# Optimization experiments

Measured on AMD Instinct MI355X. Metric: run time of the kernel, lower is better.

## Reference

```python
import jax, jax.numpy as jnp
import numpy as np

T, N, F = 8, 10000, 16
E, H, LD, ENVD = 320000, 64, 3, 5
TEMP, SAL, UI, VI = 11, 12, 13, 14
ENV_IDX = jnp.array([11, 12, 13, 14, 15])
DECAY_KM = 15.0


def _lin(k, o, i, s=0.1):
    return jax.random.normal(k, (o, i), jnp.float32) * s


def setup_inputs() -> dict:
    key = jax.random.key(0)
    ks = jax.random.split(key, 24)
    inp = {
        'node_features_sequence': jax.random.normal(ks[0], (T, N, F), jnp.float32),
        'initial_lice': jax.random.uniform(ks[1], (N, LD), jnp.float32),
        'edge_distance': jax.random.uniform(ks[2], (E,), jnp.float32) * 30.0,
        'edge_direction': jax.random.normal(ks[3], (E, 2), jnp.float32),
        'ee_w1': _lin(ks[4], H, 4), 'ee_b1': jnp.zeros((H,)),
        'ee_w2': _lin(ks[5], H, H), 'ee_b2': jnp.zeros((H,)),
        'at_w1': _lin(ks[6], H, 2 * H), 'at_b1': jnp.zeros((H,)),
        'at_w2': _lin(ks[7], 1, H), 'at_b2': jnp.zeros((1,)),
        'en_w1': _lin(ks[8], H, ENVD), 'en_b1': jnp.zeros((H,)),
        'en_w2': _lin(ks[9], H, H), 'en_b2': jnp.zeros((H,)),
        'fe_w1': _lin(ks[10], 32, 1), 'fe_b1': jnp.zeros((32,)),
        'fe_w2': _lin(ks[11], 32, 32), 'fe_b2': jnp.zeros((32,)),
        'fe_w3': _lin(ks[12], 1, 32), 'fe_b3': jnp.zeros((1,)),
        'gru_wih': _lin(ks[13], 3 * H, H + ENVD + LD),
        'gru_whh': _lin(ks[14], 3 * H, H),
        'gru_bih': jnp.zeros((3 * H,)), 'gru_bhh': jnp.zeros((3 * H,)),
        'de_w1': _lin(ks[15], H, H), 'de_b1': jnp.zeros((H,)),
        'de_w2': _lin(ks[16], LD, H), 'de_b2': jnp.zeros((LD,)),
        'log_beta': jnp.float32(-1.0),
        'temp_sensitivity': jnp.float32(0.1),
        'edge_index': jax.random.randint(ks[17], (2, E), 0, N, jnp.int32),
    }
    return inp


def _mlp2(x, w1, b1, w2, b2):
    return jax.nn.relu(x @ w1.T + b1) @ w2.T + b2


def _gru(x, h, wih, whh, bih, bhh):
    gi = x @ wih.T + bih
    gh = h @ whh.T + bhh
    i_r, i_z, i_n = jnp.split(gi, 3, axis=-1)
    h_r, h_z, h_n = jnp.split(gh, 3, axis=-1)
    r = jax.nn.sigmoid(i_r + h_r)
    z = jax.nn.sigmoid(i_z + h_z)
    n = jnp.tanh(i_n + r * h_n)
    return (1.0 - z) * n + z * h


def reference(node_features_sequence, initial_lice, edge_distance, edge_direction,
              ee_w1, ee_b1, ee_w2, ee_b2, at_w1, at_b1, at_w2, at_b2,
              en_w1, en_b1, en_w2, en_b2, fe_w1, fe_b1, fe_w2, fe_b2, fe_w3, fe_b3,
              gru_wih, gru_whh, gru_bih, gru_bhh, de_w1, de_b1, de_w2, de_b2,
              log_beta, temp_sensitivity, edge_index):
    src, dst = edge_index[0], edge_index[1]
    dist_factor = jnp.exp(-edge_distance / DECAY_KM)
    beta = jnp.exp(log_beta)

    def step(carry, x_t):
        h, lice = carry
        # dynamic edge attributes: [distance, flux+ * decay, temp_src, sal_src]
        u = x_t[src, UI]
        v = x_t[src, VI]
        flux = u * edge_direction[:, 0] + v * edge_direction[:, 1]
        wflux = jnp.clip(flux, 0.0) * dist_factor
        edge_attr = jnp.stack([edge_distance, wflux, x_t[src, TEMP], x_t[src, SAL]], axis=1)
        # edge MLP + attention logits  (E,H)
        ef = _mlp2(edge_attr, ee_w1, ee_b1, ee_w2, ee_b2)
        h_src = h[src]
        logits = _mlp2(jnp.concatenate([ef, h_src], axis=-1), at_w1, at_b1, at_w2, at_b2)[:, 0]
        logits = logits + jnp.log(wflux + 1e-8)
        # per-destination segment softmax
        amax = jax.ops.segment_max(logits, dst, num_segments=N)
        aexp = jnp.exp(logits - amax[dst])
        asum = jax.ops.segment_sum(aexp, dst, num_segments=N)
        aw = aexp / (asum[dst] + 1e-8)
        # flux-weighted lice messages, scatter-add to destinations
        weighted = (aw * lice[src, 0] * beta)[:, None] * h_src  # (E,H)
        pressure = jax.ops.segment_sum(weighted, dst, num_segments=N)  # (N,H)
        # environment + fecundity
        env = x_t[:, ENV_IDX]
        temp_norm = (x_t[:, TEMP] - 10.0) / 5.0
        fec = jax.nn.softplus(
            _mlp2(jax.nn.relu(temp_norm[:, None] @ fe_w1.T + fe_b1), fe_w2, fe_b2, fe_w3, fe_b3))[:, 0]
        env_enc = _mlp2(env, en_w1, en_b1, en_w2, en_b2)
        din = jnp.concatenate([env_enc + pressure, env, lice], axis=-1)
        h_new = _gru(din, h, gru_wih, gru_whh, gru_bih, gru_bhh)
        lice_base = jax.nn.softplus(_mlp2(h_new, de_w1, de_b1, de_w2, de_b2))
        lice_new = lice_base * (1.0 + temp_sensitivity * (fec[:, None] - 1.0))
        return (h_new, lice_new), lice_new

    h0 = jnp.zeros((N, H), jnp.float32)
    _, traj = jax.lax.scan(step, (h0, initial_lice), node_features_sequence)
    return traj  # (T, N, feature_dim)
```

## Files before the change

### kernel.cpp

```cpp
#include <hip/hip_runtime.h>
#include <math.h>

#define T_STEPS 8
#define NNODES 10000
#define NFEAT 16
#define NEDGES 320000
#define HDIM 64
#define LDIM 3
#define CAP 128

typedef _Float16 f16x8 __attribute__((ext_vector_type(8)));
typedef _Float16 f16x4 __attribute__((ext_vector_type(4)));
typedef float f32x4 __attribute__((ext_vector_type(4)));

__device__ __forceinline__ float sigmoidf_(float x){ return 1.f/(1.f+__expf(-x)); }
__device__ __forceinline__ float softplusf_(float x){ return fmaxf(x,0.f)+log1pf(__expf(-fabsf(x))); }
__device__ __forceinline__ float tanhf_(float x){ return 2.f*sigmoidf_(2.f*x)-1.f; }


__global__ void __launch_bounds__(256) k_prep(
    const float* __restrict__ ee_w2, const float* __restrict__ ee_b2,
    const float* __restrict__ at_w1, const float* __restrict__ at_b1,
    _Float16* __restrict__ P_Mhi, _Float16* __restrict__ P_Mlo,
    float* __restrict__ cvec)
{
    int i = blockIdx.x*256 + threadIdx.x;
    if (i >= 64*64) return;
    int m = i>>6, j = i&63;
    float acc = 0.f;
    #pragma unroll 8
    for (int k=0;k<64;++k) acc += ee_w2[k*64+m]*at_w1[j*128+k];
    int ks = m>>5;
    int lane = ((m>>3)&3)*16 + (j&15);
    int elem = m&7;
    int fi = (j>>4)*2 + ks;
    _Float16 hi = (_Float16)acc;
    P_Mhi[(fi*64+lane)*8+elem] = hi;
    P_Mlo[(fi*64+lane)*8+elem] = (_Float16)(acc - (float)hi);
    if (m == 0){
        float c = at_b1[j];
        #pragma unroll 8
        for (int k=0;k<64;++k) c += ee_b2[k]*at_w1[j*128+k];
        cvec[j] = c;
    }
}

__device__ __forceinline__ void packB(const float* __restrict__ W, int ldw, int koff, int K, int NKS,
                                      _Float16* __restrict__ Dhi, _Float16* __restrict__ Dlo, int li){
    int elem = li & 7;
    int lane = (li >> 3) & 63;
    int fi   = li >> 9;
    int jt = fi / NKS, ks = fi % NKS;
    int j = jt*16 + (lane & 15);
    int k = ks*32 + ((lane>>4)&3)*8 + elem;
    float v = (k < K) ? W[j*ldw + koff + k] : 0.f;
    _Float16 hi = (_Float16)v;
    Dhi[li] = hi;
    Dlo[li] = (_Float16)(v - (float)hi);
}

__global__ void __launch_bounds__(256) k_init(
    const float* __restrict__ init_lice, const float* __restrict__ cvec,
    const float* __restrict__ en_w1, const float* __restrict__ en_w2,
    const float* __restrict__ gru_wih, const float* __restrict__ gru_whh,
    const float* __restrict__ de_w1, const float* __restrict__ at_w1,
    float* __restrict__ h, float* __restrict__ lice, float* __restrict__ G,
    _Float16* __restrict__ F_en1h, _Float16* __restrict__ F_en1l,
    _Float16* __restrict__ F_enh,  _Float16* __restrict__ F_enl,
    _Float16* __restrict__ F_ihh,  _Float16* __restrict__ F_ihl,
    _Float16* __restrict__ F_hhh,  _Float16* __restrict__ F_hhl,
    _Float16* __restrict__ F_deh,  _Float16* __restrict__ F_del,
    _Float16* __restrict__ F_a2h,  _Float16* __restrict__ F_a2l,
    int* __restrict__ counts)
{
    int i = blockIdx.x*256 + threadIdx.x;
    if (i < NNODES*HDIM){ h[i] = 0.f; G[i] = cvec[i&63]; }
    if (i < NNODES*LDIM) lice[i] = init_lice[i];
    if (i < NNODES) counts[i] = 0;
    if (i < 2048)       packB(en_w1,   5,  0,  5, 1, F_en1h, F_en1l, i);
    else if (i < 6144)  packB(en_w2,  64,  0, 64, 2, F_enh,  F_enl,  i-2048);
    else if (i < 24576) packB(gru_wih,72,  0, 72, 3, F_ihh,  F_ihl,  i-6144);
    else if (i < 36864) packB(gru_whh,64,  0, 64, 2, F_hhh,  F_hhl,  i-24576);
    else if (i < 40960) packB(de_w1,  64,  0, 64, 2, F_deh,  F_del,  i-36864);
    else if (i < 45056) packB(at_w1, 128, 64, 64, 2, F_a2h,  F_a2l,  i-40960);
}

__global__ void __launch_bounds__(256) k_fec(
    const float* __restrict__ nfs,
    const float* __restrict__ fe_w1, const float* __restrict__ fe_b1,
    const float* __restrict__ fe_w2, const float* __restrict__ fe_b2,
    const float* __restrict__ fe_w3, const float* __restrict__ fe_b3,
    float* __restrict__ fec_arr)
{
    int i = blockIdx.x*256 + threadIdx.x;
    if (i >= T_STEPS*NNODES) return;
    float temp = nfs[(size_t)i*NFEAT + 11];
    float tn = (temp - 10.f)*(1.f/5.f);
    float a[32];
    #pragma unroll
    for (int k=0;k<32;++k) a[k] = fmaxf(tn*fe_w1[k] + fe_b1[k], 0.f);
    float o = fe_b3[0];
    #pragma unroll 4
    for (int l=0;l<32;++l){
        float b = fe_b2[l];
        #pragma unroll
        for (int k=0;k<32;++k) b += a[k]*fe_w2[l*32+k];
        o += fmaxf(b, 0.f)*fe_w3[l];
    }
    fec_arr[i] = softplusf_(o);
}

__global__ void __launch_bounds__(256) k_hist(const int* __restrict__ ei_dst, int* __restrict__ counts){
    int e = blockIdx.x*256 + threadIdx.x;
    if (e < NEDGES) atomicAdd(&counts[ei_dst[e]], 1);
}

__global__ void __launch_bounds__(1024) k_scan(const int* __restrict__ counts,
                                               int* __restrict__ rowptr, int* __restrict__ cursor){
    __shared__ int sums[1024];
    int t = threadIdx.x;
    const int CH = 10;
    int c0 = t*CH;
    int s = 0;
    if (c0 < NNODES){
        #pragma unroll
        for (int i=0;i<CH;i++) s += counts[c0+i];
    }
    sums[t] = s;
    __syncthreads();
    for (int off=1; off<1024; off<<=1){
        int v = (t>=off) ? sums[t-off] : 0;
        __syncthreads();
        sums[t] += v;
        __syncthreads();
    }
    if (c0 < NNODES){
        int run = (t==0) ? 0 : sums[t-1];
        for (int i=0;i<CH;i++){ rowptr[c0+i] = run; run += counts[c0+i]; cursor[c0+i] = 0; }
        if (t == (NNODES/CH)-1) rowptr[NNODES] = run;
    }
}

__global__ void __launch_bounds__(256) k_scatter(const int* __restrict__ ei_dst,
        const int* __restrict__ rowptr, int* __restrict__ cursor, int* __restrict__ perm){
    int e = blockIdx.x*256 + threadIdx.x;
    if (e >= NEDGES) return;
    int d = ei_dst[e];
    int pos = rowptr[d] + atomicAdd(&cursor[d], 1);
    perm[pos] = e;
}

__global__ void __launch_bounds__(256) k_permg(
    const int* __restrict__ perm, const int* __restrict__ ei_src,
    const float* __restrict__ dist, const float* __restrict__ dirn,
    int* __restrict__ src_perm, float* __restrict__ dist_p, float* __restrict__ dirn_p)
{
    int i = blockIdx.x*256 + threadIdx.x;
    if (i >= NEDGES) return;
    int e = perm[i];
    src_perm[i] = ei_src[e];
    dist_p[i] = dist[e];
    float2 dd = *reinterpret_cast<const float2*>(dirn + 2*e);
    *reinterpret_cast<float2*>(dirn_p + 2*i) = dd;
}


__global__ void __launch_bounds__(256,2) k_edge_mfma(
    const float* __restrict__ xt, const float* __restrict__ G,
    const int* __restrict__ src_perm,
    const float* __restrict__ dist_p, const float* __restrict__ dirn_p,
    const float* __restrict__ ee_w1, const float* __restrict__ ee_b1,
    const _Float16* __restrict__ P_Mhi, const _Float16* __restrict__ P_Mlo,
    const float* __restrict__ at_w2, const float* __restrict__ at_b2,
    float* __restrict__ logits)
{
    __shared__ __align__(16) _Float16 smh[36864];
    float* smf = (float*)smh;

    const int tid = threadIdx.x;
    const int wv = tid>>6, lane = tid&63;
    const int e = blockIdx.x*256 + tid;

    f16x8 bh[4][2], bl[4][2];
    #pragma unroll
    for (int jt=0;jt<4;++jt){
        #pragma unroll
        for (int ks=0;ks<2;++ks){
            bh[jt][ks] = *(const f16x8*)(P_Mhi + (((jt*2+ks)*64 + lane)*8));
            bl[jt][ks] = *(const f16x8*)(P_Mlo + (((jt*2+ks)*64 + lane)*8));
        }
    }

    const int src = src_perm[e];
    const float d  = dist_p[e];
    float2 dir2 = *reinterpret_cast<const float2*>(dirn_p + 2*e);
    float temp = xt[src*NFEAT+11];
    float4 q  = *reinterpret_cast<const float4*>(xt + src*NFEAT + 12);
    float flux = q.y*dir2.x + q.z*dir2.y;
    float wflux = fmaxf(flux, 0.f) * __expf(-d*(1.f/15.f));
    const float a0 = d, a1 = wflux, a2 = temp, a3 = q.x;
    const float lbias = at_b2[0] + __logf(wflux + 1e-8f);

    #pragma unroll
    for (int kb=0;kb<8;++kb){
        f16x8 hv, lv;
        #pragma unroll
        for (int i=0;i<8;++i){
            const int m = kb*8+i;
            float4 w1 = *reinterpret_cast<const float4*>(ee_w1 + m*4);
            float r = fmaxf(ee_b1[m] + a0*w1.x + a1*w1.y + a2*w1.z + a3*w1.w, 0.f);
            _Float16 hi = (_Float16)r;
            hv[i] = hi;
            lv[i] = (_Float16)(r - (float)hi);
        }
        *(f16x8*)(smh + tid*72 + kb*8)         = hv;
        *(f16x8*)(smh + 18432 + tid*72 + kb*8) = lv;
    }
    asm volatile("s_waitcnt lgkmcnt(0)" ::: "memory");

    f32x4 c[4][4];
    #pragma unroll
    for (int et=0;et<4;++et)
        #pragma unroll
        for (int jt=0;jt<4;++jt)
            c[et][jt] = (f32x4){0.f,0.f,0.f,0.f};

    #pragma unroll
    for (int et=0;et<4;++et){
        #pragma unroll
        for (int ks=0;ks<2;++ks){
            const int row = wv*64 + et*16 + (lane&15);
            f16x8 ah = *(const f16x8*)(smh + row*72 + ks*32 + (lane>>4)*8);
            f16x8 al = *(const f16x8*)(smh + 18432 + row*72 + ks*32 + (lane>>4)*8);
            #pragma unroll
            for (int jt=0;jt<4;++jt){
                c[et][jt] = __builtin_amdgcn_mfma_f32_16x16x32_f16(ah, bh[jt][ks], c[et][jt], 0,0,0);
                c[et][jt] = __builtin_amdgcn_mfma_f32_16x16x32_f16(ah, bl[jt][ks], c[et][jt], 0,0,0);
                c[et][jt] = __builtin_amdgcn_mfma_f32_16x16x32_f16(al, bh[jt][ks], c[et][jt], 0,0,0);
            }
        }
    }
    asm volatile("s_waitcnt lgkmcnt(0)" ::: "memory");

    #pragma unroll
    for (int et=0;et<4;++et){
        #pragma unroll
        for (int jt=0;jt<4;++jt){
            #pragma unroll
            for (int i=0;i<4;++i){
                const int rl = et*16 + ((lane>>4)&3)*4 + i;
                const int col = jt*16 + (lane&15);
                const int idx = (et < 2) ? (wv*2304 + rl*68 + col)
                                         : (9216 + wv*2304 + (rl-32)*68 + col);
                smf[idx] = c[et][jt][i];
            }
        }
    }
    asm volatile("s_waitcnt lgkmcnt(0)" ::: "memory");

    const int el = tid & 63;
    const float* crow = smf + ((el < 32) ? (wv*2304 + el*68)
                                         : (9216 + wv*2304 + (el-32)*68));
    const float4* G4 = reinterpret_cast<const float4*>(G + src*HDIM);
    float logit = lbias;
    #pragma unroll
    for (int jj=0;jj<16;++jj){
        float4 cv = *reinterpret_cast<const float4*>(crow + jj*4);
        float4 gv = G4[jj];
        float4 w4 = *reinterpret_cast<const float4*>(at_w2 + jj*4);
        logit += w4.x*fmaxf(cv.x+gv.x,0.f) + w4.y*fmaxf(cv.y+gv.y,0.f)
               + w4.z*fmaxf(cv.z+gv.z,0.f) + w4.w*fmaxf(cv.w+gv.w,0.f);
    }
    logits[e] = logit;
}


__global__ void __launch_bounds__(256) k_softmax_pressure(
    const float* __restrict__ logits, const float* __restrict__ h,
    const float* __restrict__ lice, const int* __restrict__ src_perm,
    const int* __restrict__ rowptr,
    const float* __restrict__ log_beta,
    float* __restrict__ pressure)
{
    __shared__ float swgt[CAP];
    __shared__ int   ssrc[CAP];
    __shared__ float sred[4][64];
    __shared__ float sredm[4], sreds[4];

    const int node = blockIdx.x;
    const int tid = threadIdx.x;
    const int wid = tid >> 6;
    const int lane = tid & 63;
    const int start = rowptr[node], end = rowptr[node+1];
    const int deg = end - start;
    const int nfast = deg < CAP ? deg : CAP;

    float m = -INFINITY;
    for (int i=start+tid; i<end; i+=256){
        float lg = logits[i];
        int o = i - start;
        if (o < CAP){ swgt[o] = lg; ssrc[o] = src_perm[i]; }
        m = fmaxf(m, lg);
    }
    #pragma unroll
    for (int off=32; off>=1; off>>=1) m = fmaxf(m, __shfl_xor(m, off));
    if (lane == 0) sredm[wid] = m;
    __syncthreads();
    m = fmaxf(fmaxf(sredm[0], sredm[1]), fmaxf(sredm[2], sredm[3]));

    float s = 0.f;
    for (int i=start+tid; i<end; i+=256){
        int o = i - start;
        float lg = (o < CAP) ? swgt[o] : logits[i];
        s += __expf(lg - m);
    }
    #pragma unroll
    for (int off=32; off>=1; off>>=1) s += __shfl_xor(s, off);
    if (lane == 0) sreds[wid] = s;
    __syncthreads();
    s = (sreds[0]+sreds[1])+(sreds[2]+sreds[3]);

    const float binv = __expf(log_beta[0])/(s + 1e-8f);

    for (int o=tid; o<nfast; o+=256){
        int sc = ssrc[o];
        swgt[o] = __expf(swgt[o] - m) * binv * lice[sc*LDIM];
    }
    __syncthreads();

    float p = 0.f;
    for (int o=wid; o<nfast; o+=4)
        p += swgt[o]*h[ssrc[o]*HDIM + lane];
    for (int i=start+CAP+wid; i<end; i+=4){
        int sc = src_perm[i];
        float wg = __expf(logits[i]-m)*binv*lice[sc*LDIM];
        p += wg*h[sc*HDIM+lane];
    }
    sred[wid][lane] = p;
    __syncthreads();
    if (wid == 0)
        pressure[node*HDIM + lane] = (sred[0][lane]+sred[1][lane])+(sred[2][lane]+sred[3][lane]);
}


__global__ void __launch_bounds__(256,4) k_node_mfma(
    const float* __restrict__ xt,
    float* __restrict__ h, float* __restrict__ lice,
    const float* __restrict__ pressure,
    const _Float16* __restrict__ F_en1h, const _Float16* __restrict__ F_en1l,
    const _Float16* __restrict__ F_enh,  const _Float16* __restrict__ F_enl,
    const _Float16* __restrict__ F_ihh,  const _Float16* __restrict__ F_ihl,
    const _Float16* __restrict__ F_hhh,  const _Float16* __restrict__ F_hhl,
    const _Float16* __restrict__ F_deh,  const _Float16* __restrict__ F_del,
    const _Float16* __restrict__ F_a2h,  const _Float16* __restrict__ F_a2l,
    const float* __restrict__ en_b1, const float* __restrict__ en_b2,
    const float* __restrict__ gru_bih, const float* __restrict__ gru_bhh,
    const float* __restrict__ de_b1, const float* __restrict__ de_w2, const float* __restrict__ de_b2,
    const float* __restrict__ cvec, const float* __restrict__ fec_t,
    const float* __restrict__ temp_sens,
    float* __restrict__ G, float* __restrict__ out_t)
{
    __shared__ __align__(16) _Float16 Ah_hi[16*72], Ah_lo[16*72];
    __shared__ __align__(16) _Float16 At_hi[16*72], At_lo[16*72];
    __shared__ __align__(16) _Float16 Ad_hi[16*104], Ad_lo[16*104];
    __shared__ float s_pd[16*64];
    __shared__ float s_fec[16];

    const int tid = threadIdx.x;
    const int w = tid>>6, lane = tid&63;
    const int l15 = lane & 15, lq = (lane>>4)&3;
    const int n0 = blockIdx.x*16;

    {
        int node = tid>>4, k4 = tid&15;
        int nc = n0 + node;
        float4 hv = *reinterpret_cast<const float4*>(h + nc*64 + k4*4);
        float4 pv = *reinterpret_cast<const float4*>(pressure + nc*64 + k4*4);
        *reinterpret_cast<float4*>(s_pd + node*64 + k4*4) = pv;
        f16x4 hh, hl;
        hh[0]=(_Float16)hv.x; hh[1]=(_Float16)hv.y; hh[2]=(_Float16)hv.z; hh[3]=(_Float16)hv.w;
        hl[0]=(_Float16)(hv.x-(float)hh[0]); hl[1]=(_Float16)(hv.y-(float)hh[1]);
        hl[2]=(_Float16)(hv.z-(float)hh[2]); hl[3]=(_Float16)(hv.w-(float)hh[3]);
        *reinterpret_cast<f16x4*>(Ah_hi + node*72 + k4*4) = hh;
        *reinterpret_cast<f16x4*>(Ah_lo + node*72 + k4*4) = hl;
    }
    if (w == 0 && lane < 16){
        int nc = n0 + lane;
        float ev[8];
        ev[0]=xt[nc*16+11]; ev[1]=xt[nc*16+12]; ev[2]=xt[nc*16+13];
        ev[3]=xt[nc*16+14]; ev[4]=xt[nc*16+15];
        ev[5]=lice[nc*3+0]; ev[6]=lice[nc*3+1]; ev[7]=lice[nc*3+2];
        s_fec[lane] = fec_t[nc];
        f16x8 eh, el;
        #pragma unroll
        for (int i=0;i<8;++i){ eh[i]=(_Float16)ev[i]; el[i]=(_Float16)(ev[i]-(float)eh[i]); }
        *reinterpret_cast<f16x8*>(Ad_hi + lane*104 + 64) = eh;
        *reinterpret_cast<f16x8*>(Ad_lo + lane*104 + 64) = el;
        f16x8 zz = {(_Float16)0,(_Float16)0,(_Float16)0,(_Float16)0,
                    (_Float16)0,(_Float16)0,(_Float16)0,(_Float16)0};
        *reinterpret_cast<f16x8*>(Ad_hi + lane*104 + 72) = zz;
        *reinterpret_cast<f16x8*>(Ad_hi + lane*104 + 80) = zz;
        *reinterpret_cast<f16x8*>(Ad_hi + lane*104 + 88) = zz;
        *reinterpret_cast<f16x8*>(Ad_lo + lane*104 + 72) = zz;
        *reinterpret_cast<f16x8*>(Ad_lo + lane*104 + 80) = zz;
        *reinterpret_cast<f16x8*>(Ad_lo + lane*104 + 88) = zz;
    }
    __syncthreads();

    {
        f16x8 bh = *(const f16x8*)(F_en1h + (w*64+lane)*8);
        f16x8 bl = *(const f16x8*)(F_en1l + (w*64+lane)*8);
        f32x4 c = (f32x4){0.f,0.f,0.f,0.f};
        f16x8 ah = *(const f16x8*)(Ad_hi + l15*104 + 64 + lq*8);
        f16x8 al = *(const f16x8*)(Ad_lo + l15*104 + 64 + lq*8);
        c = __builtin_amdgcn_mfma_f32_16x16x32_f16(ah, bh, c,0,0,0);
        c = __builtin_amdgcn_mfma_f32_16x16x32_f16(ah, bl, c,0,0,0);
        c = __builtin_amdgcn_mfma_f32_16x16x32_f16(al, bh, c,0,0,0);
        int col = w*16 + l15;
        float b1 = en_b1[col];
        #pragma unroll
        for (int i=0;i<4;++i){
            int row = lq*4 + i;
            float v = fmaxf(c[i] + b1, 0.f);
            _Float16 hi = (_Float16)v;
            At_hi[row*72+col] = hi;
            At_lo[row*72+col] = (_Float16)(v-(float)hi);
        }
    }
    __syncthreads();

    {
        f32x4 c = (f32x4){0.f,0.f,0.f,0.f};
        #pragma unroll
        for (int ks=0; ks<2; ++ks){
            f16x8 bh = *(const f16x8*)(F_enh + ((w*2+ks)*64+lane)*8);
            f16x8 bl = *(const f16x8*)(F_enl + ((w*2+ks)*64+lane)*8);
            f16x8 ah = *(const f16x8*)(At_hi + l15*72 + ks*32 + lq*8);
            f16x8 al = *(const f16x8*)(At_lo + l15*72 + ks*32 + lq*8);
            c = __builtin_amdgcn_mfma_f32_16x16x32_f16(ah, bh, c,0,0,0);
            c = __builtin_amdgcn_mfma_f32_16x16x32_f16(ah, bl, c,0,0,0);
            c = __builtin_amdgcn_mfma_f32_16x16x32_f16(al, bh, c,0,0,0);
        }
        int col = w*16 + l15;
        float b2 = en_b2[col];
        #pragma unroll
        for (int i=0;i<4;++i){
            int row = lq*4 + i;
            float v = c[i] + b2 + s_pd[row*64+col];
            _Float16 hi = (_Float16)v;
            Ad_hi[row*104+col] = hi;
            Ad_lo[row*104+col] = (_Float16)(v-(float)hi);
        }
    }
    __syncthreads();

    f32x4 Cr, Cz, Ci, Chn;
    {
        int col = w*16 + l15;
        float br = gru_bih[col]     + gru_bhh[col];
        float bz = gru_bih[64+col]  + gru_bhh[64+col];
        float bi = gru_bih[128+col];
        float bn = gru_bhh[128+col];
        Cr  = (f32x4){br,br,br,br};
        Cz  = (f32x4){bz,bz,bz,bz};
        Ci  = (f32x4){bi,bi,bi,bi};
        Chn = (f32x4){bn,bn,bn,bn};
    }
    #pragma unroll
    for (int ks=0; ks<3; ++ks){
        f16x8 ah = *(const f16x8*)(Ad_hi + l15*104 + ks*32 + lq*8);
        f16x8 al = *(const f16x8*)(Ad_lo + l15*104 + ks*32 + lq*8);
        {
            int fi = w*3 + ks;
            f16x8 bh = *(const f16x8*)(F_ihh + (fi*64+lane)*8);
            f16x8 bl = *(const f16x8*)(F_ihl + (fi*64+lane)*8);
            Cr = __builtin_amdgcn_mfma_f32_16x16x32_f16(ah, bh, Cr,0,0,0);
            Cr = __builtin_amdgcn_mfma_f32_16x16x32_f16(ah, bl, Cr,0,0,0);
            Cr = __builtin_amdgcn_mfma_f32_16x16x32_f16(al, bh, Cr,0,0,0);
        }
        {
            int fi = (4+w)*3 + ks;
            f16x8 bh = *(const f16x8*)(F_ihh + (fi*64+lane)*8);
            f16x8 bl = *(const f16x8*)(F_ihl + (fi*64+lane)*8);
            Cz = __builtin_amdgcn_mfma_f32_16x16x32_f16(ah, bh, Cz,0,0,0);
            Cz = __builtin_amdgcn_mfma_f32_16x16x32_f16(ah, bl, Cz,0,0,0);
            Cz = __builtin_amdgcn_mfma_f32_16x16x32_f16(al, bh, Cz,0,0,0);
        }
        {
            int fi = (8+w)*3 + ks;
            f16x8 bh = *(const f16x8*)(F_ihh + (fi*64+lane)*8);
            f16x8 bl = *(const f16x8*)(F_ihl + (fi*64+lane)*8);
            Ci = __builtin_amdgcn_mfma_f32_16x16x32_f16(ah, bh, Ci,0,0,0);
            Ci = __builtin_amdgcn_mfma_f32_16x16x32_f16(ah, bl, Ci,0,0,0);
            Ci = __builtin_amdgcn_mfma_f32_16x16x32_f16(al, bh, Ci,0,0,0);
        }
    }
    #pragma unroll
    for (int ks=0; ks<2; ++ks){
        f16x8 ah = *(const f16x8*)(Ah_hi + l15*72 + ks*32 + lq*8);
        f16x8 al = *(const f16x8*)(Ah_lo + l15*72 + ks*32 + lq*8);
        {
            int fi = w*2 + ks;
            f16x8 bh = *(const f16x8*)(F_hhh + (fi*64+lane)*8);
            f16x8 bl = *(const f16x8*)(F_hhl + (fi*64+lane)*8);
            Cr = __builtin_amdgcn_mfma_f32_16x16x32_f16(ah, bh, Cr,0,0,0);
            Cr = __builtin_amdgcn_mfma_f32_16x16x32_f16(ah, bl, Cr,0,0,0);
            Cr = __builtin_amdgcn_mfma_f32_16x16x32_f16(al, bh, Cr,0,0,0);
        }
        {
            int fi = (4+w)*2 + ks;
            f16x8 bh = *(const f16x8*)(F_hhh + (fi*64+lane)*8);
            f16x8 bl = *(const f16x8*)(F_hhl + (fi*64+lane)*8);
            Cz = __builtin_amdgcn_mfma_f32_16x16x32_f16(ah, bh, Cz,0,0,0);
            Cz = __builtin_amdgcn_mfma_f32_16x16x32_f16(ah, bl, Cz,0,0,0);
            Cz = __builtin_amdgcn_mfma_f32_16x16x32_f16(al, bh, Cz,0,0,0);
        }
        {
            int fi = (8+w)*2 + ks;
            f16x8 bh = *(const f16x8*)(F_hhh + (fi*64+lane)*8);
            f16x8 bl = *(const f16x8*)(F_hhl + (fi*64+lane)*8);
            Chn = __builtin_amdgcn_mfma_f32_16x16x32_f16(ah, bh, Chn,0,0,0);
            Chn = __builtin_amdgcn_mfma_f32_16x16x32_f16(ah, bl, Chn,0,0,0);
            Chn = __builtin_amdgcn_mfma_f32_16x16x32_f16(al, bh, Chn,0,0,0);
        }
    }

    float hnv[4];
    {
        const int coln = w*16 + l15;
        #pragma unroll
        for (int i=0;i<4;++i){
            int row = lq*4 + i;
            float r  = sigmoidf_(Cr[i]);
            float z  = sigmoidf_(Cz[i]);
            float nn = tanhf_(Ci[i] + r*Chn[i]);
            float hold = (float)Ah_hi[row*72+coln] + (float)Ah_lo[row*72+coln];
            hnv[i] = (1.f-z)*nn + z*hold;
        }
    }
    __syncthreads();
    {
        const int coln = w*16 + l15;
        #pragma unroll
        for (int i=0;i<4;++i){
            int row = lq*4 + i;
            float v = hnv[i];
            h[(n0+row)*HDIM + coln] = v;
            _Float16 hi = (_Float16)v;
            Ah_hi[row*72+coln] = hi;
            Ah_lo[row*72+coln] = (_Float16)(v-(float)hi);
        }
    }
    __syncthreads();

    {
        int col = w*16 + l15;
        float bd = de_b1[col], bg = cvec[col];
        f32x4 Cd = (f32x4){bd,bd,bd,bd};
        f32x4 Cg = (f32x4){bg,bg,bg,bg};
        #pragma unroll
        for (int ks=0;ks<2;++ks){
            f16x8 ah = *(const f16x8*)(Ah_hi + l15*72 + ks*32 + lq*8);
            f16x8 al = *(const f16x8*)(Ah_lo + l15*72 + ks*32 + lq*8);
            f16x8 dh = *(const f16x8*)(F_deh + ((w*2+ks)*64+lane)*8);
            f16x8 dl = *(const f16x8*)(F_del + ((w*2+ks)*64+lane)*8);
            f16x8 gh = *(const f16x8*)(F_a2h + ((w*2+ks)*64+lane)*8);
            f16x8 gl = *(const f16x8*)(F_a2l + ((w*2+ks)*64+lane)*8);
            Cd = __builtin_amdgcn_mfma_f32_16x16x32_f16(ah, dh, Cd,0,0,0);
            Cd = __builtin_amdgcn_mfma_f32_16x16x32_f16(ah, dl, Cd,0,0,0);
            Cd = __builtin_amdgcn_mfma_f32_16x16x32_f16(al, dh, Cd,0,0,0);
            Cg = __builtin_amdgcn_mfma_f32_16x16x32_f16(ah, gh, Cg,0,0,0);
            Cg = __builtin_amdgcn_mfma_f32_16x16x32_f16(ah, gl, Cg,0,0,0);
            Cg = __builtin_amdgcn_mfma_f32_16x16x32_f16(al, gh, Cg,0,0,0);
        }
        #pragma unroll
        for (int i=0;i<4;++i){
            int row = lq*4 + i;
            G[(n0+row)*HDIM + col] = Cg[i];
            s_pd[row*64+col] = fmaxf(Cd[i], 0.f);
        }
    }
    __syncthreads();

    {
        float ts = temp_sens[0];
        #pragma unroll
        for (int m=0;m<4;++m){
            int node = w*4 + m;
            float d1v = s_pd[node*64 + lane];
            float s0 = d1v*de_w2[lane];
            float s1 = d1v*de_w2[64+lane];
            float s2 = d1v*de_w2[128+lane];
            #pragma unroll
            for (int off=32; off>=1; off>>=1){
                s0 += __shfl_xor(s0,off);
                s1 += __shfl_xor(s1,off);
                s2 += __shfl_xor(s2,off);
            }
            if (lane < LDIM){
                float fec = s_fec[node];
                float oi = (lane==0?s0:(lane==1?s1:s2)) + de_b2[lane];
                float lb = softplusf_(oi);
                float ln = lb*(1.f + ts*(fec-1.f));
                lice[(n0+node)*LDIM+lane] = ln;
                out_t[(n0+node)*LDIM+lane] = ln;
            }
        }
    }
}


extern "C" void kernel_launch(void* const* d_in, const int* in_sizes, int n_in,
                              void* d_out, int out_size, void* d_ws, size_t ws_size,
                              hipStream_t stream) {
    const float* nfs       = (const float*)d_in[0];
    const float* init_lice = (const float*)d_in[1];
    const float* dist      = (const float*)d_in[2];
    const float* dirn      = (const float*)d_in[3];
    const float* ee_w1     = (const float*)d_in[4];
    const float* ee_b1     = (const float*)d_in[5];
    const float* ee_w2     = (const float*)d_in[6];
    const float* ee_b2     = (const float*)d_in[7];
    const float* at_w1     = (const float*)d_in[8];
    const float* at_b1     = (const float*)d_in[9];
    const float* at_w2     = (const float*)d_in[10];
    const float* at_b2     = (const float*)d_in[11];
    const float* en_w1     = (const float*)d_in[12];
    const float* en_b1     = (const float*)d_in[13];
    const float* en_w2     = (const float*)d_in[14];
    const float* en_b2     = (const float*)d_in[15];
    const float* fe_w1     = (const float*)d_in[16];
    const float* fe_b1     = (const float*)d_in[17];
    const float* fe_w2     = (const float*)d_in[18];
    const float* fe_b2     = (const float*)d_in[19];
    const float* fe_w3     = (const float*)d_in[20];
    const float* fe_b3     = (const float*)d_in[21];
    const float* gru_wih   = (const float*)d_in[22];
    const float* gru_whh   = (const float*)d_in[23];
    const float* gru_bih   = (const float*)d_in[24];
    const float* gru_bhh   = (const float*)d_in[25];
    const float* de_w1     = (const float*)d_in[26];
    const float* de_b1     = (const float*)d_in[27];
    const float* de_w2     = (const float*)d_in[28];
    const float* de_b2     = (const float*)d_in[29];
    const float* log_beta  = (const float*)d_in[30];
    const float* temp_sens = (const float*)d_in[31];
    const int*   ei        = (const int*)d_in[32];
    const int*   ei_src = ei;
    const int*   ei_dst = ei + NEDGES;
    float* out = (float*)d_out;

    float* wsf = (float*)d_ws;
    size_t off = 0;
    float* h        = wsf + off; off += (size_t)NNODES*HDIM;
    float* lice     = wsf + off; off += (size_t)NNODES*LDIM + 2;
    off = (off + 3) & ~(size_t)3;
    float* logits   = wsf + off; off += (size_t)NEDGES;
    float* pressure = wsf + off; off += (size_t)NNODES*HDIM;
    float* G        = wsf + off; off += (size_t)NNODES*HDIM;
    float* cvec     = wsf + off; off += 64;
    _Float16* P_Mhi = (_Float16*)(wsf + off); off += 2048;
    _Float16* P_Mlo = (_Float16*)(wsf + off); off += 2048;
    _Float16* F_en1h= (_Float16*)(wsf + off); off += 1024;
    _Float16* F_en1l= (_Float16*)(wsf + off); off += 1024;
    _Float16* F_enh = (_Float16*)(wsf + off); off += 2048;
    _Float16* F_enl = (_Float16*)(wsf + off); off += 2048;
    _Float16* F_ihh = (_Float16*)(wsf + off); off += 9216;
    _Float16* F_ihl = (_Float16*)(wsf + off); off += 9216;
    _Float16* F_hhh = (_Float16*)(wsf + off); off += 6144;
    _Float16* F_hhl = (_Float16*)(wsf + off); off += 6144;
    _Float16* F_deh = (_Float16*)(wsf + off); off += 2048;
    _Float16* F_del = (_Float16*)(wsf + off); off += 2048;
    _Float16* F_a2h = (_Float16*)(wsf + off); off += 2048;
    _Float16* F_a2l = (_Float16*)(wsf + off); off += 2048;
    float* fec_arr  = wsf + off; off += (size_t)T_STEPS*NNODES;
    float* dist_p   = wsf + off; off += NEDGES;
    float* dirn_p   = wsf + off; off += 2*NEDGES;
    int* src_perm = (int*)(wsf + off); off += NEDGES;
    int* counts = (int*)(wsf + off); off += NNODES;
    int* rowptr = (int*)(wsf + off); off += NNODES+1;
    int* cursor = (int*)(wsf + off); off += NNODES;
    int* perm   = (int*)(wsf + off); off += NEDGES;

    k_prep<<<16,256,0,stream>>>(ee_w2, ee_b2, at_w1, at_b1, P_Mhi, P_Mlo, cvec);
    k_init<<<2500,256,0,stream>>>(init_lice, cvec,
                                  en_w1, en_w2, gru_wih, gru_whh, de_w1, at_w1,
                                  h, lice, G,
                                  F_en1h, F_en1l, F_enh, F_enl,
                                  F_ihh, F_ihl, F_hhh, F_hhl,
                                  F_deh, F_del, F_a2h, F_a2l,
                                  counts);
    k_fec<<<(T_STEPS*NNODES+255)/256,256,0,stream>>>(nfs, fe_w1, fe_b1, fe_w2, fe_b2,
                                                     fe_w3, fe_b3, fec_arr);
    k_hist<<<1250,256,0,stream>>>(ei_dst, counts);
    k_scan<<<1,1024,0,stream>>>(counts, rowptr, cursor);
    k_scatter<<<1250,256,0,stream>>>(ei_dst, rowptr, cursor, perm);
    k_permg<<<1250,256,0,stream>>>(perm, ei_src, dist, dirn, src_perm, dist_p, dirn_p);

    const int node_blocks = NNODES/16;
    for (int t=0; t<T_STEPS; ++t){
        const float* xt = nfs + (size_t)t*NNODES*NFEAT;
        k_edge_mfma<<<1250,256,0,stream>>>(xt, G, src_perm, dist_p, dirn_p,
                                           ee_w1, ee_b1, P_Mhi, P_Mlo,
                                           at_w2, at_b2, logits);
        k_softmax_pressure<<<NNODES,256,0,stream>>>(logits, h, lice, src_perm,
                                                    rowptr, log_beta, pressure);
        k_node_mfma<<<node_blocks,256,0,stream>>>(xt, h, lice, pressure,
                                           F_en1h, F_en1l, F_enh, F_enl,
                                           F_ihh, F_ihl, F_hhh, F_hhl,
                                           F_deh, F_del, F_a2h, F_a2l,
                                           en_b1, en_b2, gru_bih, gru_bhh,
                                           de_b1, de_w2, de_b2,
                                           cvec, fec_arr + (size_t)t*NNODES,
                                           temp_sens,
                                           G, out + (size_t)t*NNODES*LDIM);
    }
}
```

Baseline: 756.6 us.

## Fuse softmax-pressure aggregation into node GRU kernel with ping-pong state buffers

Removes the separate per-node softmax/pressure kernel and computes each node's attention softmax and weighted neighbor aggregation inside the node MFMA kernel, with one wave handling four nodes. The h and lice state are double-buffered so the fused kernel can read the old state while writing the new one. The perm and permute-gather setup kernels are merged into the scatter kernel. This drops one launch per step and the pressure buffer round trip through global memory, but the aggregation now runs with only 625 blocks of 4 waves, which may lower parallelism and latency hiding for the gather.

```diff
diff --git a/kernel.cpp b/kernel.cpp
--- a/kernel.cpp
+++ b/kernel.cpp
@@ -7,7 +7,6 @@
 #define NEDGES 320000
 #define HDIM 64
 #define LDIM 3
-#define CAP 128
 
 typedef _Float16 f16x8 __attribute__((ext_vector_type(8)));
 typedef _Float16 f16x4 __attribute__((ext_vector_type(4)));
@@ -141,27 +140,20 @@
     }
 }
 
-__global__ void __launch_bounds__(256) k_scatter(const int* __restrict__ ei_dst,
-        const int* __restrict__ rowptr, int* __restrict__ cursor, int* __restrict__ perm){
+__global__ void __launch_bounds__(256) k_scatter(
+    const int* __restrict__ ei_src, const int* __restrict__ ei_dst,
+    const int* __restrict__ rowptr, int* __restrict__ cursor,
+    const float* __restrict__ dist, const float* __restrict__ dirn,
+    int* __restrict__ src_perm, float* __restrict__ dist_p, float* __restrict__ dirn_p)
+{
     int e = blockIdx.x*256 + threadIdx.x;
     if (e >= NEDGES) return;
     int d = ei_dst[e];
     int pos = rowptr[d] + atomicAdd(&cursor[d], 1);
-    perm[pos] = e;
-}
-
-__global__ void __launch_bounds__(256) k_permg(
-    const int* __restrict__ perm, const int* __restrict__ ei_src,
-    const float* __restrict__ dist, const float* __restrict__ dirn,
-    int* __restrict__ src_perm, float* __restrict__ dist_p, float* __restrict__ dirn_p)
-{
-    int i = blockIdx.x*256 + threadIdx.x;
-    if (i >= NEDGES) return;
-    int e = perm[i];
-    src_perm[i] = ei_src[e];
-    dist_p[i] = dist[e];
+    src_perm[pos] = ei_src[e];
+    dist_p[pos] = dist[e];
     float2 dd = *reinterpret_cast<const float2*>(dirn + 2*e);
-    *reinterpret_cast<float2*>(dirn_p + 2*i) = dd;
+    *reinterpret_cast<float2*>(dirn_p + 2*pos) = dd;
 }
 
 
@@ -275,78 +267,12 @@
 }
 
 
-__global__ void __launch_bounds__(256) k_softmax_pressure(
-    const float* __restrict__ logits, const float* __restrict__ h,
-    const float* __restrict__ lice, const int* __restrict__ src_perm,
-    const int* __restrict__ rowptr,
-    const float* __restrict__ log_beta,
-    float* __restrict__ pressure)
-{
-    __shared__ float swgt[CAP];
-    __shared__ int   ssrc[CAP];
-    __shared__ float sred[4][64];
-    __shared__ float sredm[4], sreds[4];
-
-    const int node = blockIdx.x;
-    const int tid = threadIdx.x;
-    const int wid = tid >> 6;
-    const int lane = tid & 63;
-    const int start = rowptr[node], end = rowptr[node+1];
-    const int deg = end - start;
-    const int nfast = deg < CAP ? deg : CAP;
-
-    float m = -INFINITY;
-    for (int i=start+tid; i<end; i+=256){
-        float lg = logits[i];
-        int o = i - start;
-        if (o < CAP){ swgt[o] = lg; ssrc[o] = src_perm[i]; }
-        m = fmaxf(m, lg);
-    }
-    #pragma unroll
-    for (int off=32; off>=1; off>>=1) m = fmaxf(m, __shfl_xor(m, off));
-    if (lane == 0) sredm[wid] = m;
-    __syncthreads();
-    m = fmaxf(fmaxf(sredm[0], sredm[1]), fmaxf(sredm[2], sredm[3]));
-
-    float s = 0.f;
-    for (int i=start+tid; i<end; i+=256){
-        int o = i - start;
-        float lg = (o < CAP) ? swgt[o] : logits[i];
-        s += __expf(lg - m);
-    }
-    #pragma unroll
-    for (int off=32; off>=1; off>>=1) s += __shfl_xor(s, off);
-    if (lane == 0) sreds[wid] = s;
-    __syncthreads();
-    s = (sreds[0]+sreds[1])+(sreds[2]+sreds[3]);
-
-    const float binv = __expf(log_beta[0])/(s + 1e-8f);
-
-    for (int o=tid; o<nfast; o+=256){
-        int sc = ssrc[o];
-        swgt[o] = __expf(swgt[o] - m) * binv * lice[sc*LDIM];
-    }
-    __syncthreads();
-
-    float p = 0.f;
-    for (int o=wid; o<nfast; o+=4)
-        p += swgt[o]*h[ssrc[o]*HDIM + lane];
-    for (int i=start+CAP+wid; i<end; i+=4){
-        int sc = src_perm[i];
-        float wg = __expf(logits[i]-m)*binv*lice[sc*LDIM];
-        p += wg*h[sc*HDIM+lane];
-    }
-    sred[wid][lane] = p;
-    __syncthreads();
-    if (wid == 0)
-        pressure[node*HDIM + lane] = (sred[0][lane]+sred[1][lane])+(sred[2][lane]+sred[3][lane]);
-}
-
-
-__global__ void __launch_bounds__(256,4) k_node_mfma(
+__global__ void __launch_bounds__(256,4) k_fused_node(
     const float* __restrict__ xt,
-    float* __restrict__ h, float* __restrict__ lice,
-    const float* __restrict__ pressure,
+    const float* __restrict__ h_in, float* __restrict__ h_out,
+    const float* __restrict__ lice_in, float* __restrict__ lice_out,
+    const float* __restrict__ logits, const int* __restrict__ src_perm,
+    const int* __restrict__ rowptr, const float* __restrict__ log_beta,
     const _Float16* __restrict__ F_en1h, const _Float16* __restrict__ F_en1l,
     const _Float16* __restrict__ F_enh,  const _Float16* __restrict__ F_enl,
     const _Float16* __restrict__ F_ihh,  const _Float16* __restrict__ F_ihl,
@@ -374,9 +300,7 @@
     {
         int node = tid>>4, k4 = tid&15;
         int nc = n0 + node;
-        float4 hv = *reinterpret_cast<const float4*>(h + nc*64 + k4*4);
-        float4 pv = *reinterpret_cast<const float4*>(pressure + nc*64 + k4*4);
-        *reinterpret_cast<float4*>(s_pd + node*64 + k4*4) = pv;
+        float4 hv = *reinterpret_cast<const float4*>(h_in + nc*64 + k4*4);
         f16x4 hh, hl;
         hh[0]=(_Float16)hv.x; hh[1]=(_Float16)hv.y; hh[2]=(_Float16)hv.z; hh[3]=(_Float16)hv.w;
         hl[0]=(_Float16)(hv.x-(float)hh[0]); hl[1]=(_Float16)(hv.y-(float)hh[1]);
@@ -389,7 +313,7 @@
         float ev[8];
         ev[0]=xt[nc*16+11]; ev[1]=xt[nc*16+12]; ev[2]=xt[nc*16+13];
         ev[3]=xt[nc*16+14]; ev[4]=xt[nc*16+15];
-        ev[5]=lice[nc*3+0]; ev[6]=lice[nc*3+1]; ev[7]=lice[nc*3+2];
+        ev[5]=lice_in[nc*3+0]; ev[6]=lice_in[nc*3+1]; ev[7]=lice_in[nc*3+2];
         s_fec[lane] = fec_t[nc];
         f16x8 eh, el;
         #pragma unroll
@@ -405,6 +329,48 @@
         *reinterpret_cast<f16x8*>(Ad_lo + lane*104 + 80) = zz;
         *reinterpret_cast<f16x8*>(Ad_lo + lane*104 + 88) = zz;
     }
+
+    {
+        const float beta = __expf(log_beta[0]);
+        #pragma unroll 1
+        for (int k=0;k<4;++k){
+            const int nn = w*4 + k;
+            const int n = n0 + nn;
+            const int s0 = rowptr[n], s1 = rowptr[n+1];
+
+            float m = -INFINITY;
+            for (int i=s0+lane; i<s1; i+=64) m = fmaxf(m, logits[i]);
+            #pragma unroll
+            for (int off=32; off>=1; off>>=1) m = fmaxf(m, __shfl_xor(m, off));
+
+            float s = 0.f;
+            for (int i=s0+lane; i<s1; i+=64) s += __expf(logits[i] - m);
+            #pragma unroll
+            for (int off=32; off>=1; off>>=1) s += __shfl_xor(s, off);
+
+            const float binv = beta/(s + 1e-8f);
+
+            float p0=0.f,p1=0.f,p2=0.f,p3=0.f;
+            int i = s0;
+            for (; i+4<=s1; i+=4){
+                int a0=src_perm[i+0], a1=src_perm[i+1], a2=src_perm[i+2], a3=src_perm[i+3];
+                float w0=__expf(logits[i+0]-m)*binv*lice_in[a0*LDIM];
+                float w1=__expf(logits[i+1]-m)*binv*lice_in[a1*LDIM];
+                float w2=__expf(logits[i+2]-m)*binv*lice_in[a2*LDIM];
+                float w3=__expf(logits[i+3]-m)*binv*lice_in[a3*LDIM];
+                p0 += w0*h_in[a0*HDIM+lane];
+                p1 += w1*h_in[a1*HDIM+lane];
+                p2 += w2*h_in[a2*HDIM+lane];
+                p3 += w3*h_in[a3*HDIM+lane];
+            }
+            for (; i<s1; ++i){
+                int a = src_perm[i];
+                float wg = __expf(logits[i]-m)*binv*lice_in[a*LDIM];
+                p0 += wg*h_in[a*HDIM+lane];
+            }
+            s_pd[nn*64 + lane] = (p0+p1)+(p2+p3);
+        }
+    }
     __syncthreads();
 
     {
@@ -545,7 +511,7 @@
         for (int i=0;i<4;++i){
             int row = lq*4 + i;
             float v = hnv[i];
-            h[(n0+row)*HDIM + coln] = v;
+            h_out[(n0+row)*HDIM + coln] = v;
             _Float16 hi = (_Float16)v;
             Ah_hi[row*72+coln] = hi;
             Ah_lo[row*72+coln] = (_Float16)(v-(float)hi);
@@ -602,7 +568,7 @@
                 float oi = (lane==0?s0:(lane==1?s1:s2)) + de_b2[lane];
                 float lb = softplusf_(oi);
                 float ln = lb*(1.f + ts*(fec-1.f));
-                lice[(n0+node)*LDIM+lane] = ln;
+                lice_out[(n0+node)*LDIM+lane] = ln;
                 out_t[(n0+node)*LDIM+lane] = ln;
             }
         }
@@ -652,11 +618,13 @@
 
     float* wsf = (float*)d_ws;
     size_t off = 0;
-    float* h        = wsf + off; off += (size_t)NNODES*HDIM;
-    float* lice     = wsf + off; off += (size_t)NNODES*LDIM + 2;
+    float* h0       = wsf + off; off += (size_t)NNODES*HDIM;
+    float* h1       = wsf + off; off += (size_t)NNODES*HDIM;
+    float* lice0    = wsf + off; off += (size_t)NNODES*LDIM + 2;
+    off = (off + 3) & ~(size_t)3;
+    float* lice1    = wsf + off; off += (size_t)NNODES*LDIM + 2;
     off = (off + 3) & ~(size_t)3;
     float* logits   = wsf + off; off += (size_t)NEDGES;
-    float* pressure = wsf + off; off += (size_t)NNODES*HDIM;
     float* G        = wsf + off; off += (size_t)NNODES*HDIM;
     float* cvec     = wsf + off; off += 64;
     _Float16* P_Mhi = (_Float16*)(wsf + off); off += 2048;
@@ -680,12 +648,11 @@
     int* counts = (int*)(wsf + off); off += NNODES;
     int* rowptr = (int*)(wsf + off); off += NNODES+1;
     int* cursor = (int*)(wsf + off); off += NNODES;
-    int* perm   = (int*)(wsf + off); off += NEDGES;
 
     k_prep<<<16,256,0,stream>>>(ee_w2, ee_b2, at_w1, at_b1, P_Mhi, P_Mlo, cvec);
     k_init<<<2500,256,0,stream>>>(init_lice, cvec,
                                   en_w1, en_w2, gru_wih, gru_whh, de_w1, at_w1,
-                                  h, lice, G,
+                                  h0, lice0, G,
                                   F_en1h, F_en1l, F_enh, F_enl,
                                   F_ihh, F_ihl, F_hhh, F_hhl,
                                   F_deh, F_del, F_a2h, F_a2l,
@@ -694,18 +661,21 @@
                                                      fe_w3, fe_b3, fec_arr);
     k_hist<<<1250,256,0,stream>>>(ei_dst, counts);
     k_scan<<<1,1024,0,stream>>>(counts, rowptr, cursor);
-    k_scatter<<<1250,256,0,stream>>>(ei_dst, rowptr, cursor, perm);
-    k_permg<<<1250,256,0,stream>>>(perm, ei_src, dist, dirn, src_perm, dist_p, dirn_p);
-
+    k_scatter<<<1250,256,0,stream>>>(ei_src, ei_dst, rowptr, cursor,
+                                     dist, dirn, src_perm, dist_p, dirn_p);
+
+    float* hbuf[2]    = {h0, h1};
+    float* licebuf[2] = {lice0, lice1};
     const int node_blocks = NNODES/16;
     for (int t=0; t<T_STEPS; ++t){
         const float* xt = nfs + (size_t)t*NNODES*NFEAT;
+        float* h_in  = hbuf[t&1],    *h_out = hbuf[(t+1)&1];
+        float* li_in = licebuf[t&1], *li_out = licebuf[(t+1)&1];
         k_edge_mfma<<<1250,256,0,stream>>>(xt, G, src_perm, dist_p, dirn_p,
                                            ee_w1, ee_b1, P_Mhi, P_Mlo,
                                            at_w2, at_b2, logits);
-        k_softmax_pressure<<<NNODES,256,0,stream>>>(logits, h, lice, src_perm,
-                                                    rowptr, log_beta, pressure);
-        k_node_mfma<<<node_blocks,256,0,stream>>>(xt, h, lice, pressure,
+        k_fused_node<<<node_blocks,256,0,stream>>>(xt, h_in, h_out, li_in, li_out,
+                                           logits, src_perm, rowptr, log_beta,
                                            F_en1h, F_en1l, F_enh, F_enl,
                                            F_ihh, F_ihl, F_hhh, F_hhl,
                                            F_deh, F_del, F_a2h, F_a2l,
```

New measurement: 738.5 us. 1.02x faster.
